# Optimization experiments

Measured on AMD Instinct MI355X. Metric: run time of the kernel, lower is better.

The kernel has to match this reference:

```python
import jax, jax.numpy as jnp
import numpy as np

H = 16          # num_attention_heads
D = 64          # attention_head_size
HID = 1024      # hidden_size
FF = 4096       # intermediate_size
MAXPOS = 1024   # max_position_embeddings
EPS = 1e-12     # layer_norm_eps


def _layernorm(x, g, b):
    mu = jnp.mean(x, axis=-1, keepdims=True)
    var = jnp.mean(jnp.square(x - mu), axis=-1, keepdims=True)
    return (x - mu) * jax.lax.rsqrt(var + EPS) * g + b


def setup_inputs() -> dict:
    key = jax.random.key(0)
    ks = jax.random.split(key, 16)
    B, S = 4, 1024
    std = 0.02
    inp = {
        "hidden_states": jax.random.normal(ks[0], (B, S, HID), jnp.float32),
        "attention_mask": jnp.zeros((B, 1, 1, S), jnp.float32),   # additive extended mask
        "head_mask": jnp.ones((1, H, 1, 1), jnp.float32),
        "Wq": jax.random.normal(ks[1], (HID, HID), jnp.float32) * std,
        "bq": jnp.zeros((HID,), jnp.float32),
        "Wk": jax.random.normal(ks[2], (HID, HID), jnp.float32) * std,
        "bk": jnp.zeros((HID,), jnp.float32),
        "Wv": jax.random.normal(ks[3], (HID, HID), jnp.float32) * std,
        "bv": jnp.zeros((HID,), jnp.float32),
        "dist_emb": jax.random.normal(ks[4], (2 * MAXPOS - 1, D), jnp.float32) * std,
        "Wo": jax.random.normal(ks[5], (HID, HID), jnp.float32) * std,
        "bo": jnp.zeros((HID,), jnp.float32),
        "ln1_g": jnp.ones((HID,), jnp.float32),
        "ln1_b": jnp.zeros((HID,), jnp.float32),
        "Wi": jax.random.normal(ks[6], (HID, FF), jnp.float32) * std,
        "bi": jnp.zeros((FF,), jnp.float32),
        "Wo2": jax.random.normal(ks[7], (FF, HID), jnp.float32) * std,
        "bo2": jnp.zeros((HID,), jnp.float32),
        "ln2_g": jnp.ones((HID,), jnp.float32),
        "ln2_b": jnp.zeros((HID,), jnp.float32),
    }
    return inp


def reference(hidden_states, attention_mask, head_mask, Wq, bq, Wk, bk, Wv, bv,
              dist_emb, Wo, bo, ln1_g, ln1_b, Wi, bi, Wo2, bo2, ln2_g, ln2_b):
    B, S, _ = hidden_states.shape

    def split_heads(x):  # [B,S,HID] -> [B,H,S,D]
        return x.reshape(B, S, H, D).transpose(0, 2, 1, 3)

    q = split_heads(hidden_states @ Wq + bq)
    k = split_heads(hidden_states @ Wk + bk)
    v = split_heads(hidden_states @ Wv + bv)

    # raw scores [B,H,S,S]
    scores = jnp.einsum('bhld,bhrd->bhlr', q, k)

    # relative_key_query position bias
    pos = jnp.arange(S)
    distance = pos[:, None] - pos[None, :] + (MAXPOS - 1)   # [S,S]
    pe = dist_emb[distance]                                  # [S,S,D]
    scores = scores + jnp.einsum('bhld,lrd->bhlr', q, pe) \
                    + jnp.einsum('bhrd,lrd->bhlr', k, pe)

    scores = scores / jnp.sqrt(jnp.asarray(D, scores.dtype)) + attention_mask
    probs = jax.nn.softmax(scores, axis=-1) * head_mask      # dropout p=0 (eval)

    ctx = jnp.einsum('bhlr,bhrd->bhld', probs, v)
    ctx = ctx.transpose(0, 2, 1, 3).reshape(B, S, HID)

    # RobertaSelfOutput: dense + residual LayerNorm
    attn_out = _layernorm(ctx @ Wo + bo + hidden_states, ln1_g, ln1_b)

    # RobertaIntermediate (exact GELU) + RobertaOutput
    inter = jax.nn.gelu(attn_out @ Wi + bi, approximate=False)
    out = _layernorm(inter @ Wo2 + bo2 + attn_out, ln2_g, ln2_b)
    return out
```

## Files before the change

kernel.cpp:

```cpp
#include <hip/hip_runtime.h>
#include <math.h>

typedef __attribute__((ext_vector_type(8))) short short8;
typedef __attribute__((ext_vector_type(4))) float floatx4;
typedef unsigned short u16;

#define DEVFN static __device__ __forceinline__

DEVFN float b2f(u16 u) { union { unsigned int i; float f; } x; x.i = ((unsigned int)u) << 16; return x.f; }
DEVFN u16 f2b(float f) {
    union { float f; unsigned int i; } x; x.f = f;
    unsigned int r = (x.i + 0x7fffu + ((x.i >> 16) & 1u)) >> 16;
    return (u16)r;
}

DEVFN floatx4 mfma_bf16(short8 a, short8 b, floatx4 c) {
    return __builtin_amdgcn_mfma_f32_16x16x32_bf16(a, b, c, 0, 0, 0);
}

__global__ void detect_k(const unsigned int* __restrict__ hm, int* __restrict__ flag) {
    if (threadIdx.x == 0) *flag = ((hm[0] & 0xFFFFu) != 0u) ? 1 : 0;
}

__global__ void conv_k(const void* __restrict__ src, u16* __restrict__ dst, int n,
                       const int* __restrict__ flag) {
    int i = blockIdx.x * 256 + threadIdx.x;
    if (i < n) dst[i] = (*flag) ? ((const u16*)src)[i] : f2b(((const float*)src)[i]);
}

__global__ void convT_k(const void* __restrict__ src, u16* __restrict__ dst, int R, int C,
                        const int* __restrict__ flag) {
    __shared__ u16 t[32][33];
    int bx = blockIdx.x * 32, by = blockIdx.y * 32;
    int tx = threadIdx.x, ty = threadIdx.y;
    if (*flag) {
        const u16* s = (const u16*)src;
        for (int j = ty; j < 32; j += 8) t[j][tx] = s[(size_t)(by + j) * C + bx + tx];
    } else {
        const float* s = (const float*)src;
        for (int j = ty; j < 32; j += 8) t[j][tx] = f2b(s[(size_t)(by + j) * C + bx + tx]);
    }
    __syncthreads();
    for (int j = ty; j < 32; j += 8) dst[(size_t)(bx + j) * R + by + tx] = t[tx][j];
}

template <int MODE>
__global__ __launch_bounds__(256, 2) void gemm_k(
    const u16* __restrict__ A, const u16* __restrict__ Bt,
    const u16* __restrict__ bias, const u16* __restrict__ resid,
    u16* __restrict__ Cout, int M, int N, int K) {
    __shared__ __align__(16) u16 As[128 * 40];
    __shared__ __align__(16) u16 Bs[128 * 40];
    const int m0 = blockIdx.x * 128, n0 = blockIdx.y * 128;
    const int tid = threadIdx.x;
    const int wave = tid >> 6, lane = tid & 63;
    const int wm = (wave >> 1) * 64, wn = (wave & 1) * 64;
    const int c = lane & 15, quad = lane >> 4;
    floatx4 acc[4][4] = {};
    for (int k0 = 0; k0 < K; k0 += 32) {
        __syncthreads();
        {
            int ch = tid, row = ch >> 2, kc = ch & 3;
            *(uint4*)&As[row * 40 + kc * 8] = *(const uint4*)&A[(size_t)(m0 + row) * K + k0 + kc * 8];
            *(uint4*)&Bs[row * 40 + kc * 8] = *(const uint4*)&Bt[(size_t)(n0 + row) * K + k0 + kc * 8];
            ch = tid + 256; row = ch >> 2; kc = ch & 3;
            *(uint4*)&As[row * 40 + kc * 8] = *(const uint4*)&A[(size_t)(m0 + row) * K + k0 + kc * 8];
            *(uint4*)&Bs[row * 40 + kc * 8] = *(const uint4*)&Bt[(size_t)(n0 + row) * K + k0 + kc * 8];
        }
        __syncthreads();
        short8 af[4], bf[4];
#pragma unroll
        for (int mi = 0; mi < 4; mi++) af[mi] = *(const short8*)&As[(wm + mi * 16 + c) * 40 + quad * 8];
#pragma unroll
        for (int ni = 0; ni < 4; ni++) bf[ni] = *(const short8*)&Bs[(wn + ni * 16 + c) * 40 + quad * 8];
#pragma unroll
        for (int mi = 0; mi < 4; mi++)
#pragma unroll
            for (int ni = 0; ni < 4; ni++)
                acc[mi][ni] = mfma_bf16(af[mi], bf[ni], acc[mi][ni]);
    }
#pragma unroll
    for (int ni = 0; ni < 4; ni++) {
        int col = n0 + wn + ni * 16 + c;
        float bv = b2f(bias[col]);
#pragma unroll
        for (int mi = 0; mi < 4; mi++) {
#pragma unroll
            for (int r = 0; r < 4; r++) {
                int row = m0 + wm + mi * 16 + quad * 4 + r;
                float x = acc[mi][ni][r] + bv;
                size_t idx = (size_t)row * N + col;
                if (MODE == 0) {
                    int which = col >> 10, rem = col & 1023, h = rem >> 6, d = rem & 63;
                    int bb = row >> 10, s = row & 1023;
                    Cout[(size_t)which * 4194304 + ((size_t)(bb * 16 + h) * 1024 + s) * 64 + d] = f2b(x);
                } else if (MODE == 1) {
                    Cout[idx] = f2b(x + b2f(resid[idx]));
                } else {
                    float gl = 0.5f * x * (1.0f + erff(x * 0.70710678118654752f));
                    Cout[idx] = f2b(gl);
                }
            }
        }
    }
}

__global__ __launch_bounds__(256, 2) void attn_k(
    const u16* __restrict__ q, const u16* __restrict__ k, const u16* __restrict__ v,
    const u16* __restrict__ de, const u16* __restrict__ amask, const u16* __restrict__ hmask,
    u16* __restrict__ ctx) {
    __shared__ __align__(16) u16 U1[128 * 72];
    __shared__ __align__(16) u16 Ks[64 * 72];
    __shared__ __align__(16) u16 QD[64 * 136];
    __shared__ __align__(16) u16 KD[64 * 136];
    const int bh = blockIdx.y, b = bh >> 4, h = bh & 15;
    const int L0 = blockIdx.x * 64;
    const int tid = threadIdx.x, wave = tid >> 6, lane = tid & 63;
    const int c = lane & 15, quad = lane >> 4;

    const size_t qrow = ((size_t)bh * 1024 + L0 + wave * 16 + c) * 64;
    const short8 qf0 = *(const short8*)&q[qrow + quad * 8];
    const short8 qf1 = *(const short8*)&q[qrow + 32 + quad * 8];

    floatx4 O[4] = {};
    float mrow[4] = {-1e30f, -1e30f, -1e30f, -1e30f};
    float lrow[4] = {0.f, 0.f, 0.f, 0.f};
    const float hm = b2f(hmask[h]);

    for (int rt = 0; rt < 16; rt++) {
        const int R0 = rt * 64;
        const int t0 = L0 - R0 + 960;
        __syncthreads();
        {
            int ch = tid, row = ch >> 3, kc = ch & 7;
            *(uint4*)&Ks[row * 72 + kc * 8] = *(const uint4*)&k[((size_t)bh * 1024 + R0 + row) * 64 + kc * 8];
            ch = tid + 256; row = ch >> 3; kc = ch & 7;
            *(uint4*)&Ks[row * 72 + kc * 8] = *(const uint4*)&k[((size_t)bh * 1024 + R0 + row) * 64 + kc * 8];
        }
#pragma unroll
        for (int i = 0; i < 4; i++) {
            int ch = tid + i * 256, row = ch >> 3, kc = ch & 7;
            int tr = t0 + row; if (tr > 2046) tr = 2046;
            *(uint4*)&U1[row * 72 + kc * 8] = *(const uint4*)&de[(size_t)tr * 64 + kc * 8];
        }
        __syncthreads();
#pragma unroll
        for (int ut = 0; ut < 8; ut++) {
            floatx4 a = {};
            a = mfma_bf16(qf0, *(const short8*)&U1[(ut * 16 + c) * 72 + quad * 8], a);
            a = mfma_bf16(qf1, *(const short8*)&U1[(ut * 16 + c) * 72 + 32 + quad * 8], a);
#pragma unroll
            for (int r = 0; r < 4; r++)
                QD[(wave * 16 + quad * 4 + r) * 136 + ut * 16 + c] = f2b(a[r]);
        }
        {
            short8 ka0 = *(const short8*)&Ks[(wave * 16 + c) * 72 + quad * 8];
            short8 ka1 = *(const short8*)&Ks[(wave * 16 + c) * 72 + 32 + quad * 8];
#pragma unroll
            for (int ut = 0; ut < 8; ut++) {
                floatx4 a = {};
                a = mfma_bf16(ka0, *(const short8*)&U1[(ut * 16 + c) * 72 + quad * 8], a);
                a = mfma_bf16(ka1, *(const short8*)&U1[(ut * 16 + c) * 72 + 32 + quad * 8], a);
#pragma unroll
                for (int r = 0; r < 4; r++)
                    KD[(wave * 16 + quad * 4 + r) * 136 + ut * 16 + c] = f2b(a[r]);
            }
        }
        __syncthreads();
        float sv[4][4];
#pragma unroll
        for (int nt = 0; nt < 4; nt++) {
            floatx4 a = {};
            a = mfma_bf16(qf0, *(const short8*)&Ks[(nt * 16 + c) * 72 + quad * 8], a);
            a = mfma_bf16(qf1, *(const short8*)&Ks[(nt * 16 + c) * 72 + 32 + quad * 8], a);
            int ri = nt * 16 + c;
            float am = b2f(amask[b * 1024 + R0 + ri]);
#pragma unroll
            for (int r = 0; r < 4; r++) {
                int li = wave * 16 + quad * 4 + r;
                int u = li - ri + 63;
                float biasv = b2f(QD[li * 136 + u]) + b2f(KD[ri * 136 + u]);
                sv[nt][r] = (a[r] + biasv) * 0.125f + am;
            }
        }
#pragma unroll
        for (int r = 0; r < 4; r++) {
            float rmax = fmaxf(fmaxf(sv[0][r], sv[1][r]), fmaxf(sv[2][r], sv[3][r]));
#pragma unroll
            for (int m = 1; m < 16; m <<= 1) rmax = fmaxf(rmax, __shfl_xor(rmax, m, 64));
            float mnew = fmaxf(mrow[r], rmax);
            float alpha = __expf(mrow[r] - mnew);
            float ps = 0.f;
#pragma unroll
            for (int nt = 0; nt < 4; nt++) { float p = __expf(sv[nt][r] - mnew); sv[nt][r] = p; ps += p; }
#pragma unroll
            for (int m = 1; m < 16; m <<= 1) ps += __shfl_xor(ps, m, 64);
            lrow[r] = lrow[r] * alpha + ps;
            mrow[r] = mnew;
            O[0][r] *= alpha; O[1][r] *= alpha; O[2][r] *= alpha; O[3][r] *= alpha;
        }
#pragma unroll
        for (int nt = 0; nt < 4; nt++)
#pragma unroll
            for (int r = 0; r < 4; r++)
                U1[(wave * 16 + quad * 4 + r) * 72 + nt * 16 + c] = f2b(sv[nt][r]);
        __syncthreads();
        {
            int ch = tid, row = ch >> 3, kc = ch & 7;
            uint4 raw = *(const uint4*)&v[((size_t)bh * 1024 + R0 + row) * 64 + kc * 8];
            u16 tmpv[8]; *(uint4*)tmpv = raw;
#pragma unroll
            for (int j = 0; j < 8; j++) U1[4608 + (kc * 8 + j) * 72 + row] = tmpv[j];
            ch = tid + 256; row = ch >> 3; kc = ch & 7;
            raw = *(const uint4*)&v[((size_t)bh * 1024 + R0 + row) * 64 + kc * 8];
            *(uint4*)tmpv = raw;
#pragma unroll
            for (int j = 0; j < 8; j++) U1[4608 + (kc * 8 + j) * 72 + row] = tmpv[j];
        }
        __syncthreads();
        {
            short8 pa0 = *(const short8*)&U1[(wave * 16 + c) * 72 + quad * 8];
            short8 pa1 = *(const short8*)&U1[(wave * 16 + c) * 72 + 32 + quad * 8];
#pragma unroll
            for (int dt = 0; dt < 4; dt++) {
                O[dt] = mfma_bf16(pa0, *(const short8*)&U1[4608 + (dt * 16 + c) * 72 + quad * 8], O[dt]);
                O[dt] = mfma_bf16(pa1, *(const short8*)&U1[4608 + (dt * 16 + c) * 72 + 32 + quad * 8], O[dt]);
            }
        }
    }
#pragma unroll
    for (int r = 0; r < 4; r++) {
        float inv = hm / lrow[r];
        int s = L0 + wave * 16 + quad * 4 + r;
#pragma unroll
        for (int dt = 0; dt < 4; dt++)
            ctx[(((size_t)b * 1024 + s) * 16 + h) * 64 + dt * 16 + c] = f2b(O[dt][r] * inv);
    }
}

template <int FINAL>
__global__ __launch_bounds__(256) void ln_k(const u16* __restrict__ x, const u16* __restrict__ g,
                                            const u16* __restrict__ bb, void* __restrict__ out,
                                            const int* __restrict__ flag) {
    const int row = blockIdx.x, tid = threadIdx.x;
    const u16* xr = x + (size_t)row * 1024;
    float vv[4];
#pragma unroll
    for (int j = 0; j < 4; j++) vv[j] = b2f(xr[tid * 4 + j]);
    float s = vv[0] + vv[1] + vv[2] + vv[3];
    float ss = vv[0] * vv[0] + vv[1] * vv[1] + vv[2] * vv[2] + vv[3] * vv[3];
#pragma unroll
    for (int m = 1; m < 64; m <<= 1) { s += __shfl_xor(s, m, 64); ss += __shfl_xor(ss, m, 64); }
    __shared__ float red[8];
    int wave = tid >> 6, lane = tid & 63;
    if (lane == 0) { red[wave] = s; red[wave + 4] = ss; }
    __syncthreads();
    s = red[0] + red[1] + red[2] + red[3];
    ss = red[4] + red[5] + red[6] + red[7];
    float mu = s * (1.f / 1024.f);
    float var = ss * (1.f / 1024.f) - mu * mu;
    float rs = rsqrtf(var + 1e-12f);
    const int out_bf16 = FINAL ? *flag : 1;
#pragma unroll
    for (int j = 0; j < 4; j++) {
        int idx = tid * 4 + j;
        float val = (vv[j] - mu) * rs * b2f(g[idx]) + b2f(bb[idx]);
        if (out_bf16) ((u16*)out)[(size_t)row * 1024 + idx] = f2b(val);
        else          ((float*)out)[(size_t)row * 1024 + idx] = val;
    }
}

extern "C" void kernel_launch(void* const* d_in, const int* in_sizes, int n_in,
                              void* d_out, int out_size, void* d_ws, size_t ws_size,
                              hipStream_t stream) {
    (void)in_sizes; (void)n_in; (void)out_size;
    const void* hidden = d_in[0];
    const void* amaskI = d_in[1];
    const void* hmaskI = d_in[2];
    const void* Wq = d_in[3];  const void* bq = d_in[4];
    const void* Wk = d_in[5];  const void* bk = d_in[6];
    const void* Wv = d_in[7];  const void* bv = d_in[8];
    const void* de = d_in[9];
    const void* Wo = d_in[10]; const void* bo = d_in[11];
    const void* ln1g = d_in[12]; const void* ln1b = d_in[13];
    const void* Wi = d_in[14]; const void* bi = d_in[15];
    const void* Wo2 = d_in[16]; const void* bo2 = d_in[17];
    const void* ln2g = d_in[18]; const void* ln2b = d_in[19];

    const size_t MB = 1048576;
    char* ws = (char*)d_ws;
    const bool big = (ws_size >= (size_t)70 * MB);

    u16* wsQKV  = (u16*)(ws);
    u16* wsCtx  = (u16*)(ws + 24 * MB);
    u16* wsInter= (u16*)(ws);
    u16* cHid   = (u16*)(ws + 32 * MB);
    u16* cWo2T  = (u16*)(ws + 32 * MB);
    u16* preLN  = big ? (u16*)(ws + 40 * MB) : (u16*)(ws + 16 * MB);
    u16* attnO  = big ? (u16*)(ws + 48 * MB) : (u16*)(ws + 24 * MB);
    u16* cQKVT  = big ? (u16*)(ws + 56 * MB) : (u16*)(ws + 40 * MB);
    u16* cWoT   = big ? (u16*)(ws + 62 * MB) : (u16*)(ws + 46 * MB);
    u16* cWiT   = cQKVT;
    u16* cDe    = big ? (u16*)(ws + 64 * MB) : (u16*)(ws + 48 * MB);
    u16* smalls = (u16*)((char*)cDe + 262144);
    int* flag   = (int*)((char*)smalls + 65536);

    u16* s_bqkv = smalls;
    u16* s_bo   = smalls + 3072;
    u16* s_bi   = smalls + 4096;
    u16* s_bo2  = smalls + 8192;
    u16* s_l1g  = smalls + 9216, *s_l1b = smalls + 10240;
    u16* s_l2g  = smalls + 11264, *s_l2b = smalls + 12288;
    u16* s_am   = smalls + 13312;
    u16* s_hm   = smalls + 17408;

    detect_k<<<1, 64, 0, stream>>>((const unsigned int*)hmaskI, flag);

    auto conv = [&](const void* src, u16* dst, int n) {
        conv_k<<<(n + 255) / 256, 256, 0, stream>>>(src, dst, n, flag);
    };
    auto convT = [&](const void* src, u16* dst, int R, int C) {
        convT_k<<<dim3(C / 32, R / 32), dim3(32, 8), 0, stream>>>(src, dst, R, C, flag);
    };

    conv(hidden, cHid, 4194304);
    convT(Wq, cQKVT, 1024, 1024);
    convT(Wk, cQKVT + 1048576, 1024, 1024);
    convT(Wv, cQKVT + 2097152, 1024, 1024);
    convT(Wo, cWoT, 1024, 1024);
    conv(de, cDe, 2047 * 64);
    conv(bq, s_bqkv, 1024); conv(bk, s_bqkv + 1024, 1024); conv(bv, s_bqkv + 2048, 1024);
    conv(bo, s_bo, 1024);
    conv(bi, s_bi, 4096); conv(bo2, s_bo2, 1024);
    conv(ln1g, s_l1g, 1024); conv(ln1b, s_l1b, 1024);
    conv(ln2g, s_l2g, 1024); conv(ln2b, s_l2b, 1024);
    conv(amaskI, s_am, 4096); conv(hmaskI, s_hm, 16);

    gemm_k<0><<<dim3(32, 24), 256, 0, stream>>>(cHid, cQKVT, s_bqkv, nullptr, wsQKV, 4096, 3072, 1024);

    attn_k<<<dim3(16, 64), 256, 0, stream>>>(wsQKV, wsQKV + 4194304, wsQKV + 8388608,
                                             cDe, s_am, s_hm, wsCtx);

    gemm_k<1><<<dim3(32, 8), 256, 0, stream>>>(wsCtx, cWoT, s_bo, cHid, preLN, 4096, 1024, 1024);

    convT(Wi, cWiT, 1024, 4096);
    convT(Wo2, cWo2T, 4096, 1024);

    ln_k<0><<<4096, 256, 0, stream>>>(preLN, s_l1g, s_l1b, attnO, flag);

    if (big) {
        gemm_k<2><<<dim3(32, 32), 256, 0, stream>>>(attnO, cWiT, s_bi, nullptr, wsInter, 4096, 4096, 1024);
        gemm_k<1><<<dim3(32, 8), 256, 0, stream>>>(wsInter, cWo2T, s_bo2, attnO, preLN, 4096, 1024, 4096);
    } else {
        u16* strip = (u16*)(ws);
        for (int s = 0; s < 2; s++) {
            const u16* aoff = attnO + (size_t)s * 2048 * 1024;
            gemm_k<2><<<dim3(16, 32), 256, 0, stream>>>(aoff, cWiT, s_bi, nullptr, strip, 2048, 4096, 1024);
            gemm_k<1><<<dim3(16, 8), 256, 0, stream>>>(strip, cWo2T, s_bo2, aoff,
                                                       preLN + (size_t)s * 2048 * 1024, 2048, 1024, 4096);
        }
    }

    ln_k<1><<<4096, 256, 0, stream>>>(preLN, s_l2g, s_l2b, d_out, flag);
}
```

Baseline: 612.8 us.

## Read K/V/dist-emb fragments directly from global and store V transposed

The attention kernel stops staging K, V and the distance-embedding tile through shared memory and loads MFMA operands straight from global memory. The QKV GEMM now writes V in a per-head transposed [d][s] layout, which lets PV fragments load as contiguous vectors. The relative-position bias tables are stored transposed with vectorized writes, shared memory shrinks, and the occupancy hint rises from 2 to 3 blocks. The twelve small parameter conversions are merged into one launch. The cost is more global/L2 traffic from repeated per-wave loads of K and the embedding rows.

After: 741.1 us. 1.21x slower.

```diff
diff --git a/kernel.cpp b/kernel.cpp
--- a/kernel.cpp
+++ b/kernel.cpp
@@ -26,6 +26,18 @@
                        const int* __restrict__ flag) {
     int i = blockIdx.x * 256 + threadIdx.x;
     if (i < n) dst[i] = (*flag) ? ((const u16*)src)[i] : f2b(((const float*)src)[i]);
+}
+
+struct SmallSrc { const void* p[12]; };
+__global__ void convsmall_k(SmallSrc srcs, u16* __restrict__ dst, const int* __restrict__ flag) {
+    const int offs[13] = {0, 1024, 2048, 3072, 4096, 8192, 9216, 10240, 11264, 12288, 13312, 17408, 17424};
+    int i = blockIdx.x * 256 + threadIdx.x;
+    if (i >= 17424) return;
+    int seg = 0;
+    while (i >= offs[seg + 1]) seg++;
+    int off = i - offs[seg];
+    const void* s = srcs.p[seg];
+    dst[i] = (*flag) ? ((const u16*)s)[off] : f2b(((const float*)s)[off]);
 }
 
 __global__ void convT_k(const void* __restrict__ src, u16* __restrict__ dst, int R, int C,
@@ -85,34 +97,43 @@
         float bv = b2f(bias[col]);
 #pragma unroll
         for (int mi = 0; mi < 4; mi++) {
-#pragma unroll
-            for (int r = 0; r < 4; r++) {
-                int row = m0 + wm + mi * 16 + quad * 4 + r;
-                float x = acc[mi][ni][r] + bv;
-                size_t idx = (size_t)row * N + col;
-                if (MODE == 0) {
-                    int which = col >> 10, rem = col & 1023, h = rem >> 6, d = rem & 63;
-                    int bb = row >> 10, s = row & 1023;
-                    Cout[(size_t)which * 4194304 + ((size_t)(bb * 16 + h) * 1024 + s) * 64 + d] = f2b(x);
-                } else if (MODE == 1) {
-                    Cout[idx] = f2b(x + b2f(resid[idx]));
-                } else {
-                    float gl = 0.5f * x * (1.0f + erff(x * 0.70710678118654752f));
-                    Cout[idx] = f2b(gl);
+            int row0 = m0 + wm + mi * 16 + quad * 4;
+            if (MODE == 0 && (col >> 10) == 2) {
+                int rem = col & 1023, h = rem >> 6, d = rem & 63;
+                int bb = row0 >> 10, s = row0 & 1023;
+                ushort4 pv;
+                pv.x = f2b(acc[mi][ni][0] + bv); pv.y = f2b(acc[mi][ni][1] + bv);
+                pv.z = f2b(acc[mi][ni][2] + bv); pv.w = f2b(acc[mi][ni][3] + bv);
+                *(ushort4*)&Cout[(size_t)2 * 4194304 + ((size_t)(bb * 16 + h) * 64 + d) * 1024 + s] = pv;
+            } else {
+#pragma unroll
+                for (int r = 0; r < 4; r++) {
+                    int row = row0 + r;
+                    float x = acc[mi][ni][r] + bv;
+                    size_t idx = (size_t)row * N + col;
+                    if (MODE == 0) {
+                        int which = col >> 10, rem = col & 1023, h = rem >> 6, d = rem & 63;
+                        int bb = row >> 10, s = row & 1023;
+                        Cout[(size_t)which * 4194304 + ((size_t)(bb * 16 + h) * 1024 + s) * 64 + d] = f2b(x);
+                    } else if (MODE == 1) {
+                        Cout[idx] = f2b(x + b2f(resid[idx]));
+                    } else {
+                        float gl = 0.5f * x * (1.0f + erff(x * 0.70710678118654752f));
+                        Cout[idx] = f2b(gl);
+                    }
                 }
             }
         }
     }
 }
 
-__global__ __launch_bounds__(256, 2) void attn_k(
-    const u16* __restrict__ q, const u16* __restrict__ k, const u16* __restrict__ v,
+__global__ __launch_bounds__(256, 3) void attn_k(
+    const u16* __restrict__ q, const u16* __restrict__ k, const u16* __restrict__ vt,
     const u16* __restrict__ de, const u16* __restrict__ amask, const u16* __restrict__ hmask,
     u16* __restrict__ ctx) {
-    __shared__ __align__(16) u16 U1[128 * 72];
-    __shared__ __align__(16) u16 Ks[64 * 72];
-    __shared__ __align__(16) u16 QD[64 * 136];
-    __shared__ __align__(16) u16 KD[64 * 136];
+    __shared__ __align__(16) u16 QDT[128 * 72];
+    __shared__ __align__(16) u16 KDT[128 * 72];
+    __shared__ __align__(16) u16 Ps[64 * 72];
     const int bh = blockIdx.y, b = bh >> 4, h = bh & 15;
     const int L0 = blockIdx.x * 64;
     const int tid = threadIdx.x, wave = tid >> 6, lane = tid & 63;
@@ -121,6 +142,8 @@
     const size_t qrow = ((size_t)bh * 1024 + L0 + wave * 16 + c) * 64;
     const short8 qf0 = *(const short8*)&q[qrow + quad * 8];
     const short8 qf1 = *(const short8*)&q[qrow + 32 + quad * 8];
+    const u16* kbase = k + (size_t)bh * 65536;
+    const u16* vbase = vt + (size_t)bh * 65536;
 
     floatx4 O[4] = {};
     float mrow[4] = {-1e30f, -1e30f, -1e30f, -1e30f};
@@ -130,56 +153,42 @@
     for (int rt = 0; rt < 16; rt++) {
         const int R0 = rt * 64;
         const int t0 = L0 - R0 + 960;
-        __syncthreads();
         {
-            int ch = tid, row = ch >> 3, kc = ch & 7;
-            *(uint4*)&Ks[row * 72 + kc * 8] = *(const uint4*)&k[((size_t)bh * 1024 + R0 + row) * 64 + kc * 8];
-            ch = tid + 256; row = ch >> 3; kc = ch & 7;
-            *(uint4*)&Ks[row * 72 + kc * 8] = *(const uint4*)&k[((size_t)bh * 1024 + R0 + row) * 64 + kc * 8];
-        }
-#pragma unroll
-        for (int i = 0; i < 4; i++) {
-            int ch = tid + i * 256, row = ch >> 3, kc = ch & 7;
-            int tr = t0 + row; if (tr > 2046) tr = 2046;
-            *(uint4*)&U1[row * 72 + kc * 8] = *(const uint4*)&de[(size_t)tr * 64 + kc * 8];
-        }
-        __syncthreads();
-#pragma unroll
-        for (int ut = 0; ut < 8; ut++) {
-            floatx4 a = {};
-            a = mfma_bf16(qf0, *(const short8*)&U1[(ut * 16 + c) * 72 + quad * 8], a);
-            a = mfma_bf16(qf1, *(const short8*)&U1[(ut * 16 + c) * 72 + 32 + quad * 8], a);
-#pragma unroll
-            for (int r = 0; r < 4; r++)
-                QD[(wave * 16 + quad * 4 + r) * 136 + ut * 16 + c] = f2b(a[r]);
-        }
-        {
-            short8 ka0 = *(const short8*)&Ks[(wave * 16 + c) * 72 + quad * 8];
-            short8 ka1 = *(const short8*)&Ks[(wave * 16 + c) * 72 + 32 + quad * 8];
+            const u16* krow = kbase + (size_t)(R0 + wave * 16 + c) * 64 + quad * 8;
+            const short8 ka0 = *(const short8*)krow;
+            const short8 ka1 = *(const short8*)(krow + 32);
 #pragma unroll
             for (int ut = 0; ut < 8; ut++) {
-                floatx4 a = {};
-                a = mfma_bf16(ka0, *(const short8*)&U1[(ut * 16 + c) * 72 + quad * 8], a);
-                a = mfma_bf16(ka1, *(const short8*)&U1[(ut * 16 + c) * 72 + 32 + quad * 8], a);
-#pragma unroll
-                for (int r = 0; r < 4; r++)
-                    KD[(wave * 16 + quad * 4 + r) * 136 + ut * 16 + c] = f2b(a[r]);
+                int tr = t0 + ut * 16 + c; if (tr > 2046) tr = 2046;
+                const u16* drow = de + (size_t)tr * 64 + quad * 8;
+                const short8 df0 = *(const short8*)drow;
+                const short8 df1 = *(const short8*)(drow + 32);
+                floatx4 aq = {}, ak = {};
+                aq = mfma_bf16(qf0, df0, aq); aq = mfma_bf16(qf1, df1, aq);
+                ak = mfma_bf16(ka0, df0, ak); ak = mfma_bf16(ka1, df1, ak);
+                ushort4 wq, wk;
+                wq.x = f2b(aq[0]); wq.y = f2b(aq[1]); wq.z = f2b(aq[2]); wq.w = f2b(aq[3]);
+                wk.x = f2b(ak[0]); wk.y = f2b(ak[1]); wk.z = f2b(ak[2]); wk.w = f2b(ak[3]);
+                int base = (ut * 16 + c) * 72 + wave * 16 + quad * 4;
+                *(ushort4*)&QDT[base] = wq;
+                *(ushort4*)&KDT[base] = wk;
             }
         }
         __syncthreads();
         float sv[4][4];
 #pragma unroll
         for (int nt = 0; nt < 4; nt++) {
+            const u16* ksrow = kbase + (size_t)(R0 + nt * 16 + c) * 64 + quad * 8;
             floatx4 a = {};
-            a = mfma_bf16(qf0, *(const short8*)&Ks[(nt * 16 + c) * 72 + quad * 8], a);
-            a = mfma_bf16(qf1, *(const short8*)&Ks[(nt * 16 + c) * 72 + 32 + quad * 8], a);
+            a = mfma_bf16(qf0, *(const short8*)ksrow, a);
+            a = mfma_bf16(qf1, *(const short8*)(ksrow + 32), a);
             int ri = nt * 16 + c;
             float am = b2f(amask[b * 1024 + R0 + ri]);
 #pragma unroll
             for (int r = 0; r < 4; r++) {
                 int li = wave * 16 + quad * 4 + r;
                 int u = li - ri + 63;
-                float biasv = b2f(QD[li * 136 + u]) + b2f(KD[ri * 136 + u]);
+                float biasv = b2f(QDT[u * 72 + li]) + b2f(KDT[u * 72 + ri]);
                 sv[nt][r] = (a[r] + biasv) * 0.125f + am;
             }
         }
@@ -203,28 +212,16 @@
         for (int nt = 0; nt < 4; nt++)
 #pragma unroll
             for (int r = 0; r < 4; r++)
-                U1[(wave * 16 + quad * 4 + r) * 72 + nt * 16 + c] = f2b(sv[nt][r]);
+                Ps[(wave * 16 + quad * 4 + r) * 72 + nt * 16 + c] = f2b(sv[nt][r]);
         __syncthreads();
         {
-            int ch = tid, row = ch >> 3, kc = ch & 7;
-            uint4 raw = *(const uint4*)&v[((size_t)bh * 1024 + R0 + row) * 64 + kc * 8];
-            u16 tmpv[8]; *(uint4*)tmpv = raw;
-#pragma unroll
-            for (int j = 0; j < 8; j++) U1[4608 + (kc * 8 + j) * 72 + row] = tmpv[j];
-            ch = tid + 256; row = ch >> 3; kc = ch & 7;
-            raw = *(const uint4*)&v[((size_t)bh * 1024 + R0 + row) * 64 + kc * 8];
-            *(uint4*)tmpv = raw;
-#pragma unroll
-            for (int j = 0; j < 8; j++) U1[4608 + (kc * 8 + j) * 72 + row] = tmpv[j];
-        }
-        __syncthreads();
-        {
-            short8 pa0 = *(const short8*)&U1[(wave * 16 + c) * 72 + quad * 8];
-            short8 pa1 = *(const short8*)&U1[(wave * 16 + c) * 72 + 32 + quad * 8];
+            const short8 pa0 = *(const short8*)&Ps[(wave * 16 + c) * 72 + quad * 8];
+            const short8 pa1 = *(const short8*)&Ps[(wave * 16 + c) * 72 + 32 + quad * 8];
 #pragma unroll
             for (int dt = 0; dt < 4; dt++) {
-                O[dt] = mfma_bf16(pa0, *(const short8*)&U1[4608 + (dt * 16 + c) * 72 + quad * 8], O[dt]);
-                O[dt] = mfma_bf16(pa1, *(const short8*)&U1[4608 + (dt * 16 + c) * 72 + 32 + quad * 8], O[dt]);
+                const u16* vrow = vbase + (size_t)(dt * 16 + c) * 1024 + R0 + quad * 8;
+                O[dt] = mfma_bf16(pa0, *(const short8*)vrow, O[dt]);
+                O[dt] = mfma_bf16(pa1, *(const short8*)(vrow + 32), O[dt]);
             }
         }
     }
@@ -329,12 +326,13 @@
     convT(Wv, cQKVT + 2097152, 1024, 1024);
     convT(Wo, cWoT, 1024, 1024);
     conv(de, cDe, 2047 * 64);
-    conv(bq, s_bqkv, 1024); conv(bk, s_bqkv + 1024, 1024); conv(bv, s_bqkv + 2048, 1024);
-    conv(bo, s_bo, 1024);
-    conv(bi, s_bi, 4096); conv(bo2, s_bo2, 1024);
-    conv(ln1g, s_l1g, 1024); conv(ln1b, s_l1b, 1024);
-    conv(ln2g, s_l2g, 1024); conv(ln2b, s_l2b, 1024);
-    conv(amaskI, s_am, 4096); conv(hmaskI, s_hm, 16);
+    {
+        SmallSrc st;
+        st.p[0] = bq;   st.p[1] = bk;   st.p[2] = bv;   st.p[3] = bo;
+        st.p[4] = bi;   st.p[5] = bo2;  st.p[6] = ln1g; st.p[7] = ln1b;
+        st.p[8] = ln2g; st.p[9] = ln2b; st.p[10] = amaskI; st.p[11] = hmaskI;
+        convsmall_k<<<(17424 + 255) / 256, 256, 0, stream>>>(st, smalls, flag);
+    }
 
     gemm_k<0><<<dim3(32, 24), 256, 0, stream>>>(cHid, cQKVT, s_bqkv, nullptr, wsQKV, 4096, 3072, 1024);
 
```
